# Optimization experiments

Hardware: AMD Instinct MI355X
Metric: run time of the kernel (lower is better)

Reference implementation:

```python
import jax, jax.numpy as jnp
import numpy as np

B, N, C, HF, WF = 32, 1000, 64, 12, 20
Y_DISC = 72
D = C * HF  # 768: flattened anchor feature dim (channels x fv height)


def setup_inputs() -> dict:
    key = jax.random.key(0)
    ks = jax.random.split(key, 8)
    feature_volumes = jax.random.normal(ks[0], (B, C, HF, WF), jnp.float32)
    # Anchor gather indices: channel index, row index, per-anchor x along the anchor line
    z_idx = jnp.broadcast_to(jnp.arange(C, dtype=jnp.int32)[None, :, None], (N, C, HF))
    y_idx = jnp.broadcast_to(jnp.arange(HF, dtype=jnp.int32)[None, None, :], (N, C, HF))
    x_line = jax.random.randint(ks[1], (N, 1, HF), 0, WF, dtype=jnp.int32)
    x_idx = jnp.broadcast_to(x_line, (N, C, HF))
    invalid_mask = jnp.broadcast_to(jax.random.bernoulli(ks[2], 0.2, (N, 1, HF)), (N, C, HF))
    attn_w = jax.random.normal(ks[3], (D, N - 1), jnp.float32) * 0.02
    attn_b = jnp.zeros((N - 1,), jnp.float32)
    cls_w = jax.random.normal(ks[4], (2 * D, 2), jnp.float32) * 0.02
    cls_b = jnp.zeros((2,), jnp.float32)
    reg_w = jax.random.normal(ks[5], (2 * D, Y_DISC + 1), jnp.float32) * 0.02
    reg_b = jnp.zeros((Y_DISC + 1,), jnp.float32)
    anchors_image = jax.random.normal(ks[6], (N, 5 + Y_DISC), jnp.float32)
    return {
        'feature_volumes': feature_volumes,
        'attn_w': attn_w, 'attn_b': attn_b,
        'cls_w': cls_w, 'cls_b': cls_b,
        'reg_w': reg_w, 'reg_b': reg_b,
        'anchors_image': anchors_image,
        'z_idx': z_idx, 'y_idx': y_idx, 'x_idx': x_idx,
        'invalid_mask': invalid_mask,
    }


def reference(feature_volumes, attn_w, attn_b, cls_w, cls_b, reg_w, reg_b,
              anchors_image, z_idx, y_idx, x_idx, invalid_mask):
    b = feature_volumes.shape[0]
    n = z_idx.shape[0]
    # __cut_anchor_features: gather (B, N, C, HF) rois, zero invalid entries
    rois = feature_volumes[:, z_idx, y_idx, x_idx]          # (B, N, C, HF)
    rois = jnp.where(invalid_mask[None], 0.0, rois)
    feat = rois.reshape(b, n, D)                            # (B, N, D)
    # attention layer: Linear(D -> N-1) + softmax over the N-1 dim
    scores = jax.nn.softmax(feat @ attn_w + attn_b, axis=-1)  # (B, N, N-1)
    # scatter scores into the off-diagonal of an NxN matrix (diagonal = 0)
    rows = jnp.arange(n)
    k = jnp.arange(n - 1)
    col_idx = jnp.where(k[None, :] < rows[:, None], k[None, :], k[None, :] + 1)  # (N, N-1)
    attn_mat = jnp.zeros((b, n, n), feat.dtype).at[:, rows[:, None], col_idx].set(scores)
    # bmm: attention-weighted sum of anchor features
    att_feat = jnp.einsum('bij,bjd->bid', attn_mat, feat)   # (B, N, D)
    cat = jnp.concatenate([att_feat, feat], axis=-1)        # (B, N, 2D)
    cls_logits = cat @ cls_w + cls_b                        # (B, N, 2)
    reg = cat @ reg_w + reg_b                               # (B, N, 73)
    anchors = jnp.broadcast_to(anchors_image[None], (b, n, 5 + Y_DISC))
    # proposals: [:2]=cls, [2:4]=anchor, [4:]=anchor+reg
    return jnp.concatenate([cls_logits, anchors[:, :, 2:4], anchors[:, :, 4:] + reg], axis=-1)
```

## Files before the change

kernel.cpp:

```cpp
#include <hip/hip_runtime.h>
#include <hip/hip_bf16.h>

typedef _Float16 f16;
typedef _Float16 f16x4 __attribute__((ext_vector_type(4)));
typedef _Float16 f16x8 __attribute__((ext_vector_type(8)));
typedef float    f32x4 __attribute__((ext_vector_type(4)));

static __device__ __forceinline__ float bf2f(__hip_bfloat16 x) { return __bfloat162float(x); }
static __device__ __forceinline__ float ldf(const void* p, long i, int f32flag) {
    return f32flag ? ((const float*)p)[i] : bf2f(((const __hip_bfloat16*)p)[i]);
}
static __device__ __forceinline__ void stf(void* p, long i, int f32flag, float v) {
    if (f32flag) ((float*)p)[i] = v;
    else ((__hip_bfloat16*)p)[i] = __float2bfloat16(v);
}
static __device__ __forceinline__ void gl2lds16(const f16* g, f16* l) {
    __builtin_amdgcn_global_load_lds(
        (const __attribute__((address_space(1))) unsigned int*)(const void*)g,
        (__attribute__((address_space(3))) unsigned int*)(void*)l, 16, 0, 0);
}

#define OFF_LOGITS 0L
#define SZ_LOGITS  (32000L * 1024 * 2)
#define OFF_FEAT   (OFF_LOGITS + SZ_LOGITS)
#define SZ_FEAT    (32000L * 768 * 2)
#define OFF_ATTF   (OFF_FEAT + SZ_FEAT)
#define SZ_ATTF    (32000L * 768 * 2)
#define OFF_AWT    (OFF_ATTF + SZ_ATTF)
#define SZ_AWT     (1024L * 768 * 2)
#define OFF_WCT    (OFF_AWT + SZ_AWT)
#define SZ_WCT     (128L * 1536 * 2)
#define OFF_BIAS   (OFF_WCT + SZ_WCT)
#define OFF_AB     (OFF_BIAS + 512)
#define OFF_FLAG   (OFF_AB + 4096)
#define OFF_FEATT  (OFF_FLAG + 64)
#define SZ_FEATT   (32L * 768 * 1024 * 2)
#define NEED_A     (OFF_FEATT + SZ_FEATT)

__global__ void detect_kernel(const unsigned int* __restrict__ fv,
                              const unsigned int* __restrict__ m,
                              int mwords, int* __restrict__ flags)
{
    __shared__ int cnt, bits;
    int t = threadIdx.x;
    if (t == 0) { cnt = 0; bits = 0; }
    __syncthreads();
    int c = 0;
    for (int k = t; k < 2048; k += 256) {
        unsigned int w = fv[k];
        unsigned int h0 = w & 0xffffu, h1 = w >> 16;
        unsigned int e0 = (h0 >> 7) & 0xffu, e1 = (h1 >> 7) & 0xffu;
        c += (h0 == 0u || (e0 >= 100u && e0 <= 135u)) ? 1 : 0;
        c += (h1 == 0u || (e1 >= 100u && e1 <= 135u)) ? 1 : 0;
    }
    atomicAdd(&cnt, c);
    int lb = 0;
    for (int k = t; k < mwords; k += 256) {
        unsigned int w = m[k];
        if (w > 1u) lb |= 1;
        if ((k & 1) && w != 0u) lb |= 2;
        unsigned int lo = w & 0xffffu, hi = w >> 16;
        if (!((lo == 0u || lo == 0x3f80u) && (hi == 0u || hi == 0x3f80u))) lb |= 4;
        if (lo == 0x3f80u) lb |= 8;
    }
    if (lb) atomicOr(&bits, lb);
    __syncthreads();
    if (t == 0) {
        int b = bits, f;
        if (!(b & 1))      f = (b & 2) ? 0 : 3;
        else if (!(b & 4)) f = (b & 8) ? 2 : 4;
        else               f = 1;
        flags[0] = f;
        flags[1] = (cnt < 3900) ? 1 : 0;
    }
}

__global__ __launch_bounds__(256) void build_feat_kernel(
    const void* __restrict__ fv, const int* __restrict__ x_idx,
    const void* __restrict__ maskp, const int* __restrict__ flags,
    int xstride, int mstride, f16* __restrict__ feat)
{
    __shared__ f16 sfv[15360];
    __shared__ int sx[756];
    __shared__ unsigned char sm[756];
    int b = blockIdx.y, n0 = blockIdx.x * 63;
    int rows = min(63, 1000 - n0);
    int t = threadIdx.x;
    int isf = flags[1], fm = flags[0];
    if (isf) {
        const float4* src = (const float4*)fv + (long)b * 3840;
        for (int k = t; k < 3840; k += 256) {
            float4 v = src[k];
            f16x4 h; h[0] = (f16)v.x; h[1] = (f16)v.y; h[2] = (f16)v.z; h[3] = (f16)v.w;
            *(f16x4*)&sfv[k * 4] = h;
        }
    } else {
        const uint4* src = (const uint4*)fv + (long)b * 1920;
        for (int k = t; k < 1920; k += 256) {
            uint4 v = src[k];
            unsigned int wv[4] = {v.x, v.y, v.z, v.w};
            f16x8 h;
            #pragma unroll
            for (int j = 0; j < 4; j++) {
                h[2 * j]     = (f16)__uint_as_float((wv[j] & 0xffffu) << 16);
                h[2 * j + 1] = (f16)__uint_as_float(wv[j] & 0xffff0000u);
            }
            *(f16x8*)&sfv[k * 8] = h;
        }
    }
    for (int k = t; k < rows * 12; k += 256) {
        int n = k / 12, h = k - n * 12;
        sx[k] = x_idx[(long)(n0 + n) * xstride + h];
        long mb = (long)(n0 + n) * mstride + h;
        int mv;
        if (fm == 0)      mv = ((const int*)maskp)[mb] != 0;
        else if (fm == 1) mv = ((const unsigned char*)maskp)[mb] != 0;
        else if (fm == 2) mv = ((const unsigned short*)maskp)[mb] != 0;
        else if (fm == 3) mv = ((const int*)maskp)[mb * 2] != 0;
        else              mv = ((const unsigned int*)maskp)[mb] != 0;
        sm[k] = (unsigned char)mv;
    }
    __syncthreads();
    for (int q = t; q < rows * 192; q += 256) {
        int n = q / 192, r = q - n * 192;
        int e0 = r * 4;
        f16x4 v;
        #pragma unroll
        for (int j = 0; j < 4; j++) {
            int e = e0 + j;
            int h = e % 12;
            int kk = n * 12 + h;
            v[j] = sm[kk] ? (f16)0.f : sfv[e * 20 + sx[kk]];
        }
        *(f16x4*)(feat + ((long)(b * 1000 + n0 + n)) * 768 + e0) = v;
    }
}

__global__ __launch_bounds__(256) void prep_kernel(
    const void* __restrict__ attn_w,
    const void* __restrict__ cls_w, const void* __restrict__ cls_b,
    const void* __restrict__ reg_w, const void* __restrict__ reg_b,
    const void* __restrict__ attn_b, const int* __restrict__ flags,
    f16* __restrict__ awT, f16* __restrict__ wcT,
    float* __restrict__ biasc, float* __restrict__ abf32)
{
    int isf = flags[1];
    int bid = blockIdx.x;
    int t = threadIdx.x;
    if (bid < 768) {
        __shared__ f16 tile[32][33];
        int c0 = (bid % 32) * 32, r0 = (bid / 32) * 32;
        int tx = t & 31, ty = t >> 5;
        #pragma unroll
        for (int i = ty; i < 32; i += 8) {
            int r = r0 + i, c = c0 + tx;
            float v = 0.f;
            if (r < 768 && c < 999) v = ldf(attn_w, (long)r * 999 + c, isf);
            tile[i][tx] = (f16)v;
        }
        __syncthreads();
        #pragma unroll
        for (int i = ty; i < 32; i += 8) {
            int oc = c0 + i, orw = r0 + tx;
            awT[(long)oc * 768 + orw] = tile[tx][i];
        }
    } else {
        int idx = (bid - 768) * 256 + t;
        if (idx < 128 * 1536) {
            int c = idx / 1536, k = idx - c * 1536;
            float v = 0.f;
            if (c < 2)       v = ldf(cls_w, (long)k * 2 + c, isf);
            else if (c < 75) v = ldf(reg_w, (long)k * 73 + (c - 2), isf);
            wcT[idx] = (f16)v;
        }
        if (idx < 75)
            biasc[idx] = (idx < 2) ? ldf(cls_b, idx, isf) : ldf(reg_b, idx - 2, isf);
        if (idx < 1024)
            abf32[idx] = (idx < 999) ? ldf(attn_b, idx, isf) : 0.f;
    }
}

__global__ __launch_bounds__(256) void post_kernel(
    f16* __restrict__ buf, const float* __restrict__ abf32,
    const f16* __restrict__ feat, f16* __restrict__ featT)
{
    int bid = blockIdx.x;
    int t = threadIdx.x;
    if (bid < 24576) {
        if (!featT) return;
        __shared__ f16 tile[32][33];
        int bx = bid % 24, rq = bid / 24;
        int by = rq % 32, bz = rq / 32;
        int c0 = bx * 32, r0 = by * 32;
        int tx = t & 31, ty = t >> 5;
        const f16* src = feat + (long)bz * 768000;
        #pragma unroll
        for (int i = ty; i < 32; i += 8) {
            int r = r0 + i, c = c0 + tx;
            f16 v = (f16)0.f;
            if (r < 1000) v = src[(long)r * 768 + c];
            tile[i][tx] = v;
        }
        __syncthreads();
        f16* dst = featT + (long)bz * 786432;
        #pragma unroll
        for (int i = ty; i < 32; i += 8) {
            int oc = c0 + i, orw = r0 + tx;
            dst[(long)oc * 1024 + orw] = tile[tx][i];
        }
    } else {
        int rid = bid - 24576;
        int i = rid % 1000, b = rid / 1000;
        f16* row = buf + ((long)(b * 1000 + i)) * 1024;
        __shared__ float red[8];
        int k0 = t * 4;
        f16x4 rv = *(const f16x4*)(row + k0);
        float4 ab = *(const float4*)(abf32 + k0);
        float abv[4] = {ab.x, ab.y, ab.z, ab.w};
        float v[4];
        float lmax = -3.4e38f;
        #pragma unroll
        for (int j = 0; j < 4; j++) {
            int k = k0 + j;
            float x = (k < 999) ? (float)rv[j] + abv[j] : -3.4e38f;
            v[j] = x;
            lmax = fmaxf(lmax, x);
        }
        #pragma unroll
        for (int o = 32; o > 0; o >>= 1) lmax = fmaxf(lmax, __shfl_down(lmax, o, 64));
        if ((t & 63) == 0) red[t >> 6] = lmax;
        __syncthreads();
        float gmax = fmaxf(fmaxf(red[0], red[1]), fmaxf(red[2], red[3]));
        float lsum = 0.f;
        #pragma unroll
        for (int j = 0; j < 4; j++) {
            int k = k0 + j;
            float e = (k < 999) ? __expf(v[j] - gmax) : 0.f;
            v[j] = e;
            lsum += e;
        }
        #pragma unroll
        for (int o = 32; o > 0; o >>= 1) lsum += __shfl_down(lsum, o, 64);
        if ((t & 63) == 0) red[4 + (t >> 6)] = lsum;
        __syncthreads();
        float inv = 1.f / (red[4] + red[5] + red[6] + red[7]);
        #pragma unroll
        for (int j = 0; j < 4; j++) {
            int k = k0 + j;
            if (k < 999) row[k + (k >= i ? 1 : 0)] = (f16)(v[j] * inv);
        }
        if (t == 0) row[i] = (f16)0.f;
    }
}

enum { OUT_F16 = 0, OUT_FINAL = 1 };

template<int MODE, bool CAT, bool BKM, int TM, int TN, int BK, int SWZ>
__global__ __launch_bounds__(256, 2) void gemm_kernel(
    const f16* __restrict__ A, const f16* __restrict__ A2, int lda,
    const f16* __restrict__ Bt, int ldb,
    void* __restrict__ Cout, int ldc,
    int M, int Nc, int K,
    long sA, long sB, long sC,
    const float* __restrict__ bias, const void* __restrict__ anchors,
    const int* __restrict__ flags)
{
    int t = threadIdx.x;
    int bx, by, bz;
    if constexpr (SWZ == 2) {
        int bid = blockIdx.x;
        int xcd = bid & 7, s = bid >> 3;
        int g = xcd + 8 * (s >> 2);
        if (g >= (M + TM - 1) / TM) return;
        by = g; bx = s & 3; bz = 0;
    } else if constexpr (SWZ == 3) {
        int bid = blockIdx.x;
        int xcd = bid & 7, s = bid >> 3;
        bz = xcd * 4 + s / 24;
        int wv = s % 24;
        by = wv / 3; bx = wv - by * 3;
    } else { bx = blockIdx.x; by = blockIdx.y; bz = blockIdx.z; }

    int m0 = by * TM, n0 = bx * TN;
    int z = bz;
    A  += (long)z * sA;
    if (CAT) A2 += (long)z * sA;
    Bt += (long)z * sB;
    int w = t >> 6, lane = t & 63;
    constexpr int NJ = (TM == 128 && TN == 256) ? 8 : ((TN == 256) ? 4 : ((TM == 128) ? 4 : 2));
    int wm = (TM == 128) ? (w & 1) * 64 : 0;
    int wn;
    if constexpr (TM == 128 && TN == 256) wn = (w >> 1) * 128;
    else if constexpr (TN == 256)         wn = w * 64;
    else if constexpr (TM == 128)         wn = (w >> 1) * 64;
    else                                  wn = w * 32;

    int lr = lane & 15, lq = lane >> 4;

    const f32x4 zero4 = {0.f, 0.f, 0.f, 0.f};
    f32x4 acc[4][NJ];
    #pragma unroll
    for (int i = 0; i < 4; i++)
        #pragma unroll
        for (int j = 0; j < NJ; j++) acc[i][j] = zero4;

    if constexpr (!BKM) {
        constexpr int CH  = BK / 8;
        constexpr int AI  = TM * BK / 2048;
        constexpr int BI  = TN * BK / 2048;
        constexpr int RPO = 2048 / BK;
        __shared__ __align__(16) f16 As[TM * BK];
        __shared__ __align__(16) f16 Bs[TN * BK];
        int row0 = t / CH, slot = t % CH;
        int csw = slot ^ (row0 & (CH - 1));
        long aoffB = (long)(m0 + row0) * lda + csw * 8;
        long boffB = (long)(n0 + row0) * ldb + csw * 8;
        for (int k0 = 0; k0 < K; k0 += BK) {
            const f16* Ak = A; int kk = k0;
            if (CAT && k0 >= 768) { Ak = A2; kk = k0 - 768; }
            __syncthreads();
            #pragma unroll
            for (int i = 0; i < AI; i++)
                gl2lds16(Ak + aoffB + (long)(i * RPO) * lda + kk, &As[i * 2048 + w * 512]);
            #pragma unroll
            for (int i = 0; i < BI; i++)
                gl2lds16(Bt + boffB + (long)(i * RPO) * ldb + k0, &Bs[i * 2048 + w * 512]);
            __syncthreads();
            #pragma unroll
            for (int ks = 0; ks < BK / 32; ks++) {
                f16x8 af[4], bfr[NJ];
                #pragma unroll
                for (int i = 0; i < 4; i++) {
                    int r = wm + i * 16 + lr;
                    int cc = (lq + ks * 4) ^ (r & (CH - 1));
                    af[i] = *(const f16x8*)&As[r * BK + cc * 8];
                }
                #pragma unroll
                for (int j = 0; j < NJ; j++) {
                    int r = wn + j * 16 + lr;
                    int cc = (lq + ks * 4) ^ (r & (CH - 1));
                    bfr[j] = *(const f16x8*)&Bs[r * BK + cc * 8];
                }
                #pragma unroll
                for (int i = 0; i < 4; i++)
                    #pragma unroll
                    for (int j = 0; j < NJ; j++)
                        acc[i][j] = __builtin_amdgcn_mfma_f32_16x16x32_f16(af[i], bfr[j], acc[i][j], 0, 0, 0);
            }
        }
    } else {
        __shared__ __align__(16) f16 As[128 * 40];
        __shared__ __align__(16) f16 Bs[32 * 132];
        const f16x8 zero8 = {(f16)0, (f16)0, (f16)0, (f16)0, (f16)0, (f16)0, (f16)0, (f16)0};
        const f16x4 zero4h = {(f16)0, (f16)0, (f16)0, (f16)0};
        for (int k0 = 0; k0 < K; k0 += 32) {
            __syncthreads();
            #pragma unroll
            for (int i = 0; i < 2; i++) {
                int q = t + i * 256;
                { int row = q >> 2, kc = (q & 3) * 8;
                  f16x8 av = zero8;
                  if ((m0 + row) < M && (k0 + kc) < K)
                      av = *(const f16x8*)(A + (long)(m0 + row) * lda + k0 + kc);
                  *(f16x8*)&As[row * 40 + kc] = av; }
                { int kr = q >> 4, nc = (q & 15) * 8;
                  f16x4 b0 = zero4h, b1 = zero4h;
                  if ((k0 + kr) < K && (n0 + nc) < Nc) {
                      const f16* p2 = Bt + (long)(k0 + kr) * ldb + n0 + nc;
                      b0 = *(const f16x4*)p2;
                      b1 = *(const f16x4*)(p2 + 4);
                  }
                  *(f16x4*)&Bs[kr * 132 + nc]     = b0;
                  *(f16x4*)&Bs[kr * 132 + nc + 4] = b1; }
            }
            __syncthreads();
            f16x8 af[4], bfr[NJ];
            #pragma unroll
            for (int i = 0; i < 4; i++)
                af[i] = *(const f16x8*)&As[(wm + i * 16 + lr) * 40 + lq * 8];
            #pragma unroll
            for (int j = 0; j < NJ; j++)
                #pragma unroll
                for (int jj = 0; jj < 8; jj++)
                    bfr[j][jj] = Bs[(lq * 8 + jj) * 132 + wn + j * 16 + lr];
            #pragma unroll
            for (int i = 0; i < 4; i++)
                #pragma unroll
                for (int j = 0; j < NJ; j++)
                    acc[i][j] = __builtin_amdgcn_mfma_f32_16x16x32_f16(af[i], bfr[j], acc[i][j], 0, 0, 0);
        }
    }

    int isf = (MODE == OUT_FINAL) ? flags[1] : 0;
    #pragma unroll
    for (int i = 0; i < 4; i++) {
        #pragma unroll
        for (int j = 0; j < NJ; j++) {
            #pragma unroll
            for (int r = 0; r < 4; r++) {
                int gm = m0 + wm + i * 16 + lq * 4 + r;
                int gn = n0 + wn + j * 16 + lr;
                if (MODE == OUT_F16) {
                    if (gm < M && gn < Nc)
                        ((f16*)Cout)[(long)z * sC + (long)gm * ldc + gn] = (f16)acc[i][j][r];
                } else {
                    if (gn < Nc) {
                        float v = acc[i][j][r] + bias[gn];
                        int oc = (gn < 2) ? gn : gn + 2;
                        if (gn >= 2) v += ldf(anchors, (long)(gm % 1000) * 77 + oc, isf);
                        stf(Cout, (long)gm * 77 + oc, isf, v);
                    } else if (gn < 77) {
                        int oc = gn - 73;
                        stf(Cout, (long)gm * 77 + oc, isf,
                            ldf(anchors, (long)(gm % 1000) * 77 + oc, isf));
                    }
                }
            }
        }
    }
}

extern "C" void kernel_launch(void* const* d_in, const int* in_sizes, int n_in,
                              void* d_out, int out_size, void* d_ws, size_t ws_size,
                              hipStream_t stream)
{
    const void* fv      = d_in[0];
    const void* attn_w  = d_in[1];
    const void* attn_b  = d_in[2];
    const void* cls_w   = d_in[3];
    const void* cls_b   = d_in[4];
    const void* reg_w   = d_in[5];
    const void* reg_b   = d_in[6];
    const void* anchors = d_in[7];
    const int*  x_idx   = (const int*)d_in[10];
    const void* maskp   = d_in[11];
    int xstride = (in_sizes[10] < 768000) ? 12 : 768;
    int mstride = (in_sizes[11] < 768000) ? 12 : 768;
    int mwords  = in_sizes[11] / 4;
    if (mwords > 4096) mwords = 4096;

    char* ws = (char*)d_ws;
    f16*   logits = (f16*)(ws + OFF_LOGITS);
    f16*   feat   = (f16*)(ws + OFF_FEAT);
    f16*   attf   = (f16*)(ws + OFF_ATTF);
    f16*   awT    = (f16*)(ws + OFF_AWT);
    f16*   wcT    = (f16*)(ws + OFF_WCT);
    float* biasc  = (float*)(ws + OFF_BIAS);
    float* abf32  = (float*)(ws + OFF_AB);
    int*   flags  = (int*)(ws + OFF_FLAG);
    f16*   featT  = (f16*)(ws + OFF_FEATT);
    bool bigws = ws_size >= (size_t)NEED_A;

    detect_kernel<<<dim3(1), dim3(256), 0, stream>>>(
        (const unsigned int*)fv, (const unsigned int*)maskp, mwords, flags);
    build_feat_kernel<<<dim3(16, 32), dim3(256), 0, stream>>>(
        fv, x_idx, maskp, flags, xstride, mstride, feat);
    prep_kernel<<<dim3(1536), dim3(256), 0, stream>>>(
        attn_w, cls_w, cls_b, reg_w, reg_b, attn_b, flags, awT, wcT, biasc, abf32);

    gemm_kernel<OUT_F16, false, false, 128, 256, 64, 2><<<dim3(1024), dim3(256), 0, stream>>>(
        feat, nullptr, 768, awT, 768, logits, 1024, 32000, 1024, 768, 0, 0, 0,
        nullptr, nullptr, flags);
    post_kernel<<<dim3(24576 + 32000), dim3(256), 0, stream>>>(
        logits, abf32, feat, bigws ? featT : nullptr);
    if (bigws) {
        gemm_kernel<OUT_F16, false, false, 128, 256, 64, 3><<<dim3(768), dim3(256), 0, stream>>>(
            logits, nullptr, 1024, featT, 1024, attf, 768, 1000, 768, 1024,
            1024000L, 786432L, 768000L, nullptr, nullptr, flags);
    } else {
        gemm_kernel<OUT_F16, false, true, 128, 128, 32, 0><<<dim3(6, 8, 32), dim3(256), 0, stream>>>(
            logits, nullptr, 1024, feat, 768, attf, 768, 1000, 768, 1000,
            1024000L, 768000L, 768000L, nullptr, nullptr, flags);
    }
    gemm_kernel<OUT_FINAL, true, false, 64, 128, 128, 0><<<dim3(1, 500, 1), dim3(256), 0, stream>>>(
        attf, feat, 768, wcT, 1536, d_out, 77, 32000, 75, 1536, 0, 0, 0,
        biasc, anchors, flags);
}
```

Measured before the change: 347.6 us.

## Merge feature build and weight prep kernels; load final-GEMM B operand directly to registers

```diff
diff --git a/kernel.cpp b/kernel.cpp
--- a/kernel.cpp
+++ b/kernel.cpp
@@ -75,81 +75,77 @@
     }
 }
 
-__global__ __launch_bounds__(256) void build_feat_kernel(
+__global__ __launch_bounds__(256) void front_kernel(
     const void* __restrict__ fv, const int* __restrict__ x_idx,
     const void* __restrict__ maskp, const int* __restrict__ flags,
-    int xstride, int mstride, f16* __restrict__ feat)
-{
-    __shared__ f16 sfv[15360];
-    __shared__ int sx[756];
-    __shared__ unsigned char sm[756];
-    int b = blockIdx.y, n0 = blockIdx.x * 63;
-    int rows = min(63, 1000 - n0);
-    int t = threadIdx.x;
-    int isf = flags[1], fm = flags[0];
-    if (isf) {
-        const float4* src = (const float4*)fv + (long)b * 3840;
-        for (int k = t; k < 3840; k += 256) {
-            float4 v = src[k];
-            f16x4 h; h[0] = (f16)v.x; h[1] = (f16)v.y; h[2] = (f16)v.z; h[3] = (f16)v.w;
-            *(f16x4*)&sfv[k * 4] = h;
-        }
-    } else {
-        const uint4* src = (const uint4*)fv + (long)b * 1920;
-        for (int k = t; k < 1920; k += 256) {
-            uint4 v = src[k];
-            unsigned int wv[4] = {v.x, v.y, v.z, v.w};
-            f16x8 h;
-            #pragma unroll
-            for (int j = 0; j < 4; j++) {
-                h[2 * j]     = (f16)__uint_as_float((wv[j] & 0xffffu) << 16);
-                h[2 * j + 1] = (f16)__uint_as_float(wv[j] & 0xffff0000u);
-            }
-            *(f16x8*)&sfv[k * 8] = h;
-        }
-    }
-    for (int k = t; k < rows * 12; k += 256) {
-        int n = k / 12, h = k - n * 12;
-        sx[k] = x_idx[(long)(n0 + n) * xstride + h];
-        long mb = (long)(n0 + n) * mstride + h;
-        int mv;
-        if (fm == 0)      mv = ((const int*)maskp)[mb] != 0;
-        else if (fm == 1) mv = ((const unsigned char*)maskp)[mb] != 0;
-        else if (fm == 2) mv = ((const unsigned short*)maskp)[mb] != 0;
-        else if (fm == 3) mv = ((const int*)maskp)[mb * 2] != 0;
-        else              mv = ((const unsigned int*)maskp)[mb] != 0;
-        sm[k] = (unsigned char)mv;
-    }
-    __syncthreads();
-    for (int q = t; q < rows * 192; q += 256) {
-        int n = q / 192, r = q - n * 192;
-        int e0 = r * 4;
-        f16x4 v;
-        #pragma unroll
-        for (int j = 0; j < 4; j++) {
-            int e = e0 + j;
-            int h = e % 12;
-            int kk = n * 12 + h;
-            v[j] = sm[kk] ? (f16)0.f : sfv[e * 20 + sx[kk]];
-        }
-        *(f16x4*)(feat + ((long)(b * 1000 + n0 + n)) * 768 + e0) = v;
-    }
-}
-
-__global__ __launch_bounds__(256) void prep_kernel(
+    int xstride, int mstride, f16* __restrict__ feat,
     const void* __restrict__ attn_w,
     const void* __restrict__ cls_w, const void* __restrict__ cls_b,
     const void* __restrict__ reg_w, const void* __restrict__ reg_b,
-    const void* __restrict__ attn_b, const int* __restrict__ flags,
+    const void* __restrict__ attn_b,
     f16* __restrict__ awT, f16* __restrict__ wcT,
     float* __restrict__ biasc, float* __restrict__ abf32)
 {
-    int isf = flags[1];
     int bid = blockIdx.x;
     int t = threadIdx.x;
-    if (bid < 768) {
+    int isf = flags[1], fm = flags[0];
+    if (bid < 512) {
+        __shared__ f16 sfv[15360];
+        __shared__ int sx[756];
+        __shared__ unsigned char sm[756];
+        int b = bid >> 4, n0 = (bid & 15) * 63;
+        int rows = min(63, 1000 - n0);
+        if (isf) {
+            const float4* src = (const float4*)fv + (long)b * 3840;
+            for (int k = t; k < 3840; k += 256) {
+                float4 v = src[k];
+                f16x4 h; h[0] = (f16)v.x; h[1] = (f16)v.y; h[2] = (f16)v.z; h[3] = (f16)v.w;
+                *(f16x4*)&sfv[k * 4] = h;
+            }
+        } else {
+            const uint4* src = (const uint4*)fv + (long)b * 1920;
+            for (int k = t; k < 1920; k += 256) {
+                uint4 v = src[k];
+                unsigned int wv[4] = {v.x, v.y, v.z, v.w};
+                f16x8 h;
+                #pragma unroll
+                for (int j = 0; j < 4; j++) {
+                    h[2 * j]     = (f16)__uint_as_float((wv[j] & 0xffffu) << 16);
+                    h[2 * j + 1] = (f16)__uint_as_float(wv[j] & 0xffff0000u);
+                }
+                *(f16x8*)&sfv[k * 8] = h;
+            }
+        }
+        for (int k = t; k < rows * 12; k += 256) {
+            int n = k / 12, h = k - n * 12;
+            sx[k] = x_idx[(long)(n0 + n) * xstride + h];
+            long mb = (long)(n0 + n) * mstride + h;
+            int mv;
+            if (fm == 0)      mv = ((const int*)maskp)[mb] != 0;
+            else if (fm == 1) mv = ((const unsigned char*)maskp)[mb] != 0;
+            else if (fm == 2) mv = ((const unsigned short*)maskp)[mb] != 0;
+            else if (fm == 3) mv = ((const int*)maskp)[mb * 2] != 0;
+            else              mv = ((const unsigned int*)maskp)[mb] != 0;
+            sm[k] = (unsigned char)mv;
+        }
+        __syncthreads();
+        for (int q = t; q < rows * 192; q += 256) {
+            int n = q / 192, r = q - n * 192;
+            int e0 = r * 4;
+            f16x4 v;
+            #pragma unroll
+            for (int j = 0; j < 4; j++) {
+                int e = e0 + j;
+                int h = e % 12;
+                int kk = n * 12 + h;
+                v[j] = sm[kk] ? (f16)0.f : sfv[e * 20 + sx[kk]];
+            }
+            *(f16x4*)(feat + ((long)(b * 1000 + n0 + n)) * 768 + e0) = v;
+        }
+    } else if (bid < 1280) {
         __shared__ f16 tile[32][33];
-        int c0 = (bid % 32) * 32, r0 = (bid / 32) * 32;
+        int tid = bid - 512;
+        int c0 = (tid % 32) * 32, r0 = (tid / 32) * 32;
         int tx = t & 31, ty = t >> 5;
         #pragma unroll
         for (int i = ty; i < 32; i += 8) {
@@ -165,7 +161,7 @@
             awT[(long)oc * 768 + orw] = tile[tx][i];
         }
     } else {
-        int idx = (bid - 768) * 256 + t;
+        int idx = (bid - 1280) * 256 + t;
         if (idx < 128 * 1536) {
             int c = idx / 1536, k = idx - c * 1536;
             float v = 0.f;
@@ -255,7 +251,7 @@
 
 enum { OUT_F16 = 0, OUT_FINAL = 1 };
 
-template<int MODE, bool CAT, bool BKM, int TM, int TN, int BK, int SWZ>
+template<int MODE, bool CAT, bool BKM, int TM, int TN, int BK, int SWZ, bool BG>
 __global__ __launch_bounds__(256, 2) void gemm_kernel(
     const f16* __restrict__ A, const f16* __restrict__ A2, int lda,
     const f16* __restrict__ Bt, int ldb,
@@ -304,7 +300,47 @@
         #pragma unroll
         for (int j = 0; j < NJ; j++) acc[i][j] = zero4;
 
-    if constexpr (!BKM) {
+    if constexpr (BG) {
+        constexpr int CH  = BK / 8;
+        constexpr int AI  = TM * BK / 2048;
+        constexpr int RPO = 2048 / BK;
+        __shared__ __align__(16) f16 As[TM * BK];
+        int row0 = t / CH, slot = t % CH;
+        int csw = slot ^ (row0 & (CH - 1));
+        long aoffB = (long)(m0 + row0) * lda + csw * 8;
+        for (int k0 = 0; k0 < K; k0 += BK) {
+            const f16* Ak = A; int kk = k0;
+            if (CAT && k0 >= 768) { Ak = A2; kk = k0 - 768; }
+            __syncthreads();
+            #pragma unroll
+            for (int i = 0; i < AI; i++)
+                gl2lds16(Ak + aoffB + (long)(i * RPO) * lda + kk, &As[i * 2048 + w * 512]);
+            f16x8 ball[BK / 32][NJ];
+            #pragma unroll
+            for (int ks = 0; ks < BK / 32; ks++)
+                #pragma unroll
+                for (int j = 0; j < NJ; j++) {
+                    int r = wn + j * 16 + lr;
+                    ball[ks][j] = *(const f16x8*)(Bt + (long)r * ldb + k0 + (ks * 4 + lq) * 8);
+                }
+            __syncthreads();
+            #pragma unroll
+            for (int ks = 0; ks < BK / 32; ks++) {
+                f16x8 af[4];
+                #pragma unroll
+                for (int i = 0; i < 4; i++) {
+                    int r = wm + i * 16 + lr;
+                    int cc = (lq + ks * 4) ^ (r & (CH - 1));
+                    af[i] = *(const f16x8*)&As[r * BK + cc * 8];
+                }
+                #pragma unroll
+                for (int i = 0; i < 4; i++)
+                    #pragma unroll
+                    for (int j = 0; j < NJ; j++)
+                        acc[i][j] = __builtin_amdgcn_mfma_f32_16x16x32_f16(af[i], ball[ks][j], acc[i][j], 0, 0, 0);
+            }
+        }
+    } else if constexpr (!BKM) {
         constexpr int CH  = BK / 8;
         constexpr int AI  = TM * BK / 2048;
         constexpr int BI  = TN * BK / 2048;
@@ -453,26 +489,25 @@
 
     detect_kernel<<<dim3(1), dim3(256), 0, stream>>>(
         (const unsigned int*)fv, (const unsigned int*)maskp, mwords, flags);
-    build_feat_kernel<<<dim3(16, 32), dim3(256), 0, stream>>>(
-        fv, x_idx, maskp, flags, xstride, mstride, feat);
-    prep_kernel<<<dim3(1536), dim3(256), 0, stream>>>(
-        attn_w, cls_w, cls_b, reg_w, reg_b, attn_b, flags, awT, wcT, biasc, abf32);
-
-    gemm_kernel<OUT_F16, false, false, 128, 256, 64, 2><<<dim3(1024), dim3(256), 0, stream>>>(
+    front_kernel<<<dim3(2048), dim3(256), 0, stream>>>(
+        fv, x_idx, maskp, flags, xstride, mstride, feat,
+        attn_w, cls_w, cls_b, reg_w, reg_b, attn_b, awT, wcT, biasc, abf32);
+
+    gemm_kernel<OUT_F16, false, false, 128, 256, 64, 2, false><<<dim3(1024), dim3(256), 0, stream>>>(
         feat, nullptr, 768, awT, 768, logits, 1024, 32000, 1024, 768, 0, 0, 0,
         nullptr, nullptr, flags);
     post_kernel<<<dim3(24576 + 32000), dim3(256), 0, stream>>>(
         logits, abf32, feat, bigws ? featT : nullptr);
     if (bigws) {
-        gemm_kernel<OUT_F16, false, false, 128, 256, 64, 3><<<dim3(768), dim3(256), 0, stream>>>(
+        gemm_kernel<OUT_F16, false, false, 128, 256, 64, 3, false><<<dim3(768), dim3(256), 0, stream>>>(
             logits, nullptr, 1024, featT, 1024, attf, 768, 1000, 768, 1024,
             1024000L, 786432L, 768000L, nullptr, nullptr, flags);
     } else {
-        gemm_kernel<OUT_F16, false, true, 128, 128, 32, 0><<<dim3(6, 8, 32), dim3(256), 0, stream>>>(
+        gemm_kernel<OUT_F16, false, true, 128, 128, 32, 0, false><<<dim3(6, 8, 32), dim3(256), 0, stream>>>(
             logits, nullptr, 1024, feat, 768, attf, 768, 1000, 768, 1000,
             1024000L, 768000L, 768000L, nullptr, nullptr, flags);
     }
-    gemm_kernel<OUT_FINAL, true, false, 64, 128, 128, 0><<<dim3(1, 500, 1), dim3(256), 0, stream>>>(
+    gemm_kernel<OUT_FINAL, true, false, 64, 128, 128, 0, true><<<dim3(1, 500, 1), dim3(256), 0, stream>>>(
         attf, feat, 768, wcT, 1536, d_out, 77, 32000, 75, 1536, 0, 0, 0,
         biasc, anchors, flags);
 }
```

Measured after the change: 340.9 us. About the same (-1.9%).
